# Kernel tuning notes

Measured on AMD Instinct MI355X. Metric: run time of the kernel, lower is better.

Reference implementation:

```python
import jax, jax.numpy as jnp
import numpy as np

B, C, H, W = 8, 320, 64, 64      # query feature map
S_KV, D_KV = 77, 1024            # key/value (text) tokens
HEADS, DIM_HEAD = 8, 64
INNER = HEADS * DIM_HEAD         # 512


def setup_inputs() -> dict:
    key = jax.random.key(0)
    ks = jax.random.split(key, 7)
    return {
        "query": jax.random.normal(ks[0], (B, C, H, W), dtype=jnp.float32),
        "key_value": jax.random.normal(ks[1], (B, S_KV, D_KV), dtype=jnp.float32),
        "Wq": jax.random.normal(ks[2], (C, INNER), dtype=jnp.float32) * (C ** -0.5),
        "Wk": jax.random.normal(ks[3], (D_KV, INNER), dtype=jnp.float32) * (D_KV ** -0.5),
        "Wv": jax.random.normal(ks[4], (D_KV, INNER), dtype=jnp.float32) * (D_KV ** -0.5),
        "Wo": jax.random.normal(ks[5], (INNER, C), dtype=jnp.float32) * (INNER ** -0.5),
        "bo": jnp.zeros((C,), dtype=jnp.float32),
    }


def reference(query, key_value, Wq, Wk, Wv, Wo, bo):
    b, c, h, w = query.shape
    n = h * w
    # [B,C,H,W] -> [B,N,C]
    q_flat = query.reshape(b, c, n).transpose(0, 2, 1)
    # projections, then split heads: [B, S, heads, dim_head]
    q = (q_flat @ Wq).reshape(b, n, HEADS, DIM_HEAD)
    k = (key_value @ Wk).reshape(b, S_KV, HEADS, DIM_HEAD)
    v = (key_value @ Wv).reshape(b, S_KV, HEADS, DIM_HEAD)
    scale = DIM_HEAD ** -0.5
    # attn logits: [B, heads, N, S_kv]
    logits = jnp.einsum('bnhd,bshd->bhns', q, k) * scale
    attn = jax.nn.softmax(logits, axis=-1)
    # weighted values -> merge heads: [B, N, inner]
    out = jnp.einsum('bhns,bshd->bnhd', attn, v).reshape(b, n, INNER)
    out = out @ Wo + bo  # dropout p=0.0 is identity
    # [B,N,C] -> [B,C,H,W]
    return out.transpose(0, 2, 1).reshape(b, c, h, w)
```

## Files before the change

### kernel.cpp

```cpp
#include <hip/hip_runtime.h>
#include <hip/hip_bf16.h>
#include <stdint.h>

#define BB     8
#define CC     320
#define NN     4096
#define SKV    77
#define HEADS  8
#define INNER  512
#define SCALE  0.125f

typedef float f32x4  __attribute__((ext_vector_type(4)));
typedef short bf16x8 __attribute__((ext_vector_type(8)));
typedef short s16x4  __attribute__((ext_vector_type(4)));

static __device__ __forceinline__ short f2bf(float f) {
  unsigned u = __float_as_uint(f);
  return (short)((u + 0x7fffu + ((u >> 16) & 1u)) >> 16);
}

static __device__ __forceinline__ void gll16(void* lds, const void* g) {
  auto gp = reinterpret_cast<const uint32_t __attribute__((address_space(1)))*>(
      reinterpret_cast<uintptr_t>(g));
  auto lp = reinterpret_cast<uint32_t __attribute__((address_space(3)))*>(
      reinterpret_cast<uintptr_t>(lds));
  __builtin_amdgcn_global_load_lds(gp, lp, 16, 0, 0);
}

__global__ __launch_bounds__(256) void prep_kernel(
    const float* __restrict__ kv, const float* __restrict__ Wk,
    const float* __restrict__ Wv, const float* __restrict__ Wq,
    const float* __restrict__ Wo, const float* __restrict__ query,
    short* __restrict__ kv_bf, short* __restrict__ Wk_t,
    short* __restrict__ Wv_t, short* __restrict__ Wq_t,
    short* __restrict__ Wo_t, short* __restrict__ X_bf,
    unsigned* __restrict__ zero_base) {
  __shared__ float T[64 * 65];
  const int blk = blockIdx.x, t = threadIdx.x;
  if (blk < 616) {
    const int base = blk * 1024;
    #pragma unroll
    for (int i = 0; i < 4; ++i) kv_bf[base + i*256 + t] = f2bf(kv[base + i*256 + t]);
    return;
  }
  if (blk >= 1392) {
    const int blk2 = blk - 1392;
    const int b = blk2 / 320, r = blk2 % 320;
    const int nt = r / 5, ct = r % 5;
    const int tl = t & 63, rb = t >> 6;
    #pragma unroll
    for (int i = 0; i < 16; ++i) {
      const int c = rb + i*4;
      T[c*65 + tl] = query[((size_t)(b*CC + ct*64 + c))*NN + nt*64 + tl];
    }
    __syncthreads();
    #pragma unroll
    for (int i = 0; i < 16; ++i) {
      const int n = rb + i*4;
      X_bf[((size_t)(b*NN + nt*64 + n))*CC + ct*64 + tl] = f2bf(T[tl*65 + n]);
    }
    return;
  }
  if (blk >= 952) {
    const int base = (blk - 952) * 1024;
    #pragma unroll
    for (int i = 0; i < 4; ++i) zero_base[base + i*256 + t] = 0u;
    return;
  }
  const float* src; short* dst; int RS, CS, kt, ct; float scl = 1.0f;
  if (blk < 872) {
    const int tile = blk - 616;
    const bool isK = tile < 128;
    const int tt = isK ? tile : tile - 128;
    src = isK ? Wk : Wv; dst = isK ? Wk_t : Wv_t;
    RS = 1024; CS = 512; kt = tt >> 3; ct = tt & 7;
  } else if (blk < 912) {
    const int tt = blk - 872;
    src = Wq; dst = Wq_t; RS = 320; CS = 512; kt = tt >> 3; ct = tt & 7;
    scl = SCALE;
  } else {
    const int tt = blk - 912;
    src = Wo; dst = Wo_t; RS = 512; CS = 320; kt = tt / 5; ct = tt % 5;
  }
  const int cl = t & 63, rb = t >> 6;
  #pragma unroll
  for (int i = 0; i < 16; ++i)
    T[(rb + i*4)*65 + cl] = src[(size_t)(kt*64 + rb + i*4)*CS + ct*64 + cl];
  __syncthreads();
  #pragma unroll
  for (int i = 0; i < 16; ++i) {
    const int nl = rb + i*4;
    dst[(size_t)(ct*64 + nl)*RS + kt*64 + cl] = f2bf(T[cl*65 + nl] * scl);
  }
}

__global__ __launch_bounds__(256) void kvproj_kernel(
    const short* __restrict__ kv_bf, const short* __restrict__ Wk_t,
    const short* __restrict__ Wv_t, short* __restrict__ K_ws,
    short* __restrict__ V_ws) {
  const int t = threadIdx.x, w = t >> 6, lane = t & 63;
  const int l15 = lane & 15, q = lane >> 4;
  const int m0 = (blockIdx.x * 4 + w) * 16;
  const int y = blockIdx.y;
  const bool isK = (y < 8);
  const int h = y & 7;
  const short* __restrict__ Wt = isK ? Wk_t : Wv_t;
  const int arow = (m0 + l15 < 616) ? (m0 + l15) : 615;

  const f32x4 z = {0.f, 0.f, 0.f, 0.f};
  f32x4 acc[4] = {z, z, z, z};
  for (int k0 = 0; k0 < 1024; k0 += 32) {
    const bf16x8 a = *(const bf16x8*)(kv_bf + arow*1024 + k0 + q*8);
    #pragma unroll
    for (int nt = 0; nt < 4; ++nt) {
      const int n = h*64 + nt*16 + l15;
      const bf16x8 bfr = *(const bf16x8*)(Wt + n*1024 + k0 + q*8);
      acc[nt] = __builtin_amdgcn_mfma_f32_16x16x32_bf16(a, bfr, acc[nt], 0, 0, 0);
    }
  }
  #pragma unroll
  for (int nt = 0; nt < 4; ++nt) {
    const int d = nt*16 + l15;
    #pragma unroll
    for (int r = 0; r < 4; ++r) {
      const int row = m0 + q*4 + r;
      if (row < 616) {
        const int b = (int)(((unsigned)row * 54472u) >> 22);
        const int s = row - b*77;
        if (isK) K_ws[((b*8 + h)*80 + s)*64 + d] = f2bf(acc[nt][r]);
        else     V_ws[((b*8 + h)*64 + d)*96 + s] = f2bf(acc[nt][r]);
      }
    }
  }
}

__global__ __launch_bounds__(256, 2) void qproj_kernel(
    const short* __restrict__ X_bf, const short* __restrict__ Wq_t,
    short* __restrict__ Q_ws) {
  const int t = threadIdx.x, w = t >> 6, lane = t & 63;
  const int l15 = lane & 15, q = lane >> 4;
  const int m0 = (blockIdx.x >> 1) * 128;
  const int n0 = (blockIdx.x & 1) * 256;
  const int wm = w & 1, wn = w >> 1;

  __shared__ short tile[12288];

  const f32x4 z = {0.f, 0.f, 0.f, 0.f};
  f32x4 acc[4][8];
  #pragma unroll
  for (int mt = 0; mt < 4; ++mt)
    #pragma unroll
    for (int nt = 0; nt < 8; ++nt) acc[mt][nt] = z;

  for (int it = 0; it < 10; ++it) {
    const int k0 = it * 32;
    if (it) __syncthreads();
    #pragma unroll
    for (int p = 0; p < 2; ++p) {
      const int f = p*256 + t, row = f >> 2, c4 = f & 3;
      gll16(tile + f*8, X_bf + (size_t)(m0 + row)*320 + k0 + c4*8);
    }
    #pragma unroll
    for (int p = 0; p < 4; ++p) {
      const int f = p*256 + t, row = f >> 2, c4 = f & 3;
      gll16(tile + 4096 + f*8, Wq_t + (size_t)(n0 + row)*320 + k0 + c4*8);
    }
    __syncthreads();
    bf16x8 a[4], bb[8];
    #pragma unroll
    for (int mt = 0; mt < 4; ++mt)
      a[mt] = *(const bf16x8*)(tile + (wm*64 + mt*16 + l15)*32 + q*8);
    #pragma unroll
    for (int nt = 0; nt < 8; ++nt)
      bb[nt] = *(const bf16x8*)(tile + 4096 + (wn*128 + nt*16 + l15)*32 + q*8);
    #pragma unroll
    for (int mt = 0; mt < 4; ++mt)
      #pragma unroll
      for (int nt = 0; nt < 8; ++nt)
        acc[mt][nt] = __builtin_amdgcn_mfma_f32_16x16x32_bf16(a[mt], bb[nt], acc[mt][nt], 0, 0, 0);
  }
  #pragma unroll
  for (int mt = 0; mt < 4; ++mt)
    #pragma unroll
    for (int r = 0; r < 4; ++r) {
      short* rowp = Q_ws + (size_t)(m0 + wm*64 + mt*16 + q*4 + r)*512 + n0 + wn*128;
      #pragma unroll
      for (int nt = 0; nt < 8; ++nt)
        rowp[nt*16 + l15] = f2bf(acc[mt][nt][r]);
    }
}

__global__ __launch_bounds__(256) void attncore_kernel(
    const short* __restrict__ Q_ws, const short* __restrict__ K_ws,
    const short* __restrict__ V_ws, short* __restrict__ O_ws) {
  const int t = threadIdx.x, w = t >> 6, lane = t & 63;
  const int unit = blockIdx.x * 4 + w;
  const int h = unit & 7;
  const int g = unit >> 3;
  const int b = g >> 7;
  const int n0 = (g & 127) * 32;
  const int l15 = lane & 15, q = lane >> 4;

  __shared__ short scr[4 * 32 * 104];
  short* scrw = scr + w * 32 * 104;
  for (int i = lane; i < 32*104/2; i += 64) ((unsigned*)scrw)[i] = 0u;

  const short* __restrict__ Kh = K_ws + (size_t)(b*8 + h) * 80 * 64;
  const short* __restrict__ Vh = V_ws + (size_t)(b*8 + h) * 64 * 96;
  size_t tokrow[2];
  #pragma unroll
  for (int nt = 0; nt < 2; ++nt) tokrow[nt] = (size_t)(b*NN + n0 + nt*16 + l15);

  const f32x4 z = {0.f, 0.f, 0.f, 0.f};
  f32x4 qk[2][5];
  #pragma unroll
  for (int nt = 0; nt < 2; ++nt)
    #pragma unroll
    for (int st = 0; st < 5; ++st) qk[nt][st] = z;
  #pragma unroll
  for (int f = 0; f < 2; ++f) {
    bf16x8 bq[2];
    #pragma unroll
    for (int nt = 0; nt < 2; ++nt)
      bq[nt] = *(const bf16x8*)(Q_ws + tokrow[nt]*512 + h*64 + f*32 + q*8);
    #pragma unroll
    for (int st = 0; st < 5; ++st) {
      const bf16x8 a = *(const bf16x8*)(Kh + (st*16 + l15)*64 + f*32 + q*8);
      #pragma unroll
      for (int nt = 0; nt < 2; ++nt)
        qk[nt][st] = __builtin_amdgcn_mfma_f32_16x16x32_bf16(a, bq[nt], qk[nt][st], 0, 0, 0);
    }
  }

  #pragma unroll
  for (int nt = 0; nt < 2; ++nt) {
    float mx = -1e30f;
    #pragma unroll
    for (int st = 0; st < 5; ++st)
      #pragma unroll
      for (int r = 0; r < 4; ++r) {
        const int s = st*16 + q*4 + r;
        const float vv = (s < SKV) ? qk[nt][st][r] : -1e30f;
        qk[nt][st][r] = vv;
        mx = fmaxf(mx, vv);
      }
    mx = fmaxf(mx, __shfl_xor(mx, 16));
    mx = fmaxf(mx, __shfl_xor(mx, 32));
    float sum = 0.f;
    #pragma unroll
    for (int st = 0; st < 5; ++st)
      #pragma unroll
      for (int r = 0; r < 4; ++r) {
        const int s = st*16 + q*4 + r;
        const float e = (s < SKV) ? __expf(qk[nt][st][r] - mx) : 0.f;
        qk[nt][st][r] = e;
        sum += e;
      }
    sum += __shfl_xor(sum, 16);
    sum += __shfl_xor(sum, 32);
    const float inv = 1.0f / sum;
    #pragma unroll
    for (int st = 0; st < 5; ++st) {
      s16x4 pv;
      #pragma unroll
      for (int r = 0; r < 4; ++r) pv[r] = f2bf(qk[nt][st][r] * inv);
      *(s16x4*)(scrw + (nt*16 + l15)*104 + st*16 + q*4) = pv;
    }
  }

  f32x4 ov[2][4];
  #pragma unroll
  for (int nt = 0; nt < 2; ++nt)
    #pragma unroll
    for (int dt = 0; dt < 4; ++dt) ov[nt][dt] = z;
  #pragma unroll
  for (int f = 0; f < 3; ++f) {
    bf16x8 bp[2];
    #pragma unroll
    for (int nt = 0; nt < 2; ++nt)
      bp[nt] = *(const bf16x8*)(scrw + (nt*16 + l15)*104 + f*32 + q*8);
    #pragma unroll
    for (int dt = 0; dt < 4; ++dt) {
      const bf16x8 a = *(const bf16x8*)(Vh + (dt*16 + l15)*96 + f*32 + q*8);
      #pragma unroll
      for (int nt = 0; nt < 2; ++nt)
        ov[nt][dt] = __builtin_amdgcn_mfma_f32_16x16x32_bf16(a, bp[nt], ov[nt][dt], 0, 0, 0);
    }
  }
  #pragma unroll
  for (int nt = 0; nt < 2; ++nt)
    #pragma unroll
    for (int dt = 0; dt < 4; ++dt) {
      s16x4 pv;
      #pragma unroll
      for (int r = 0; r < 4; ++r) pv[r] = f2bf(ov[nt][dt][r]);
      *(s16x4*)(O_ws + tokrow[nt]*512 + h*64 + dt*16 + q*4) = pv;
    }
}

__global__ __launch_bounds__(256) void outproj_kernel(
    const short* __restrict__ O_ws, const short* __restrict__ Wo_t,
    const float* __restrict__ bo, float* __restrict__ out) {
  const int t = threadIdx.x, w = t >> 6, lane = t & 63;
  const int l15 = lane & 15, q = lane >> 4;
  const int c0 = (blockIdx.x & 1) * 160;
  const int t0 = (blockIdx.x >> 1) * 128;
  const int wm = w & 1, wn = w >> 1;

  __shared__ short tile[9216];

  const f32x4 z = {0.f, 0.f, 0.f, 0.f};
  f32x4 acc[5][4];
  #pragma unroll
  for (int mt = 0; mt < 5; ++mt)
    #pragma unroll
    for (int nt = 0; nt < 4; ++nt) acc[mt][nt] = z;

  for (int it = 0; it < 16; ++it) {
    const int k0 = it * 32;
    if (it) __syncthreads();
    #pragma unroll
    for (int p = 0; p < 5; ++p) {
      const int f = p*256 + t;
      if (f < 1152) {
        const short* g;
        if (f < 640) {
          const int row = f >> 2, c4 = f & 3;
          g = Wo_t + (size_t)(c0 + row)*512 + k0 + c4*8;
        } else {
          const int f2 = f - 640, row = f2 >> 2, c4 = f2 & 3;
          g = O_ws + (size_t)(t0 + row)*512 + k0 + c4*8;
        }
        gll16(tile + f*8, g);
      }
    }
    __syncthreads();
    bf16x8 a[5], bb[4];
    #pragma unroll
    for (int mt = 0; mt < 5; ++mt)
      a[mt] = *(const bf16x8*)(tile + (wm*80 + mt*16 + l15)*32 + q*8);
    #pragma unroll
    for (int nt = 0; nt < 4; ++nt)
      bb[nt] = *(const bf16x8*)(tile + 5120 + (wn*64 + nt*16 + l15)*32 + q*8);
    #pragma unroll
    for (int mt = 0; mt < 5; ++mt)
      #pragma unroll
      for (int nt = 0; nt < 4; ++nt)
        acc[mt][nt] = __builtin_amdgcn_mfma_f32_16x16x32_bf16(a[mt], bb[nt], acc[mt][nt], 0, 0, 0);
  }
  const int b = t0 >> 12, n = t0 & 4095;
  #pragma unroll
  for (int mt = 0; mt < 5; ++mt)
    #pragma unroll
    for (int r = 0; r < 4; ++r) {
      const int c = c0 + wm*80 + mt*16 + q*4 + r;
      const float bv = bo[c];
      float* rowp = out + ((size_t)(b*CC + c))*NN + n + wn*64;
      #pragma unroll
      for (int nt = 0; nt < 4; ++nt)
        rowp[nt*16 + l15] = acc[mt][nt][r] + bv;
    }
}

extern "C" void kernel_launch(void* const* d_in, const int* in_sizes, int n_in,
                              void* d_out, int out_size, void* d_ws, size_t ws_size,
                              hipStream_t stream) {
  const float* query = (const float*)d_in[0];
  const float* kv    = (const float*)d_in[1];
  const float* Wq    = (const float*)d_in[2];
  const float* Wk    = (const float*)d_in[3];
  const float* Wv    = (const float*)d_in[4];
  const float* Wo    = (const float*)d_in[5];
  const float* bo    = (const float*)d_in[6];
  float* out = (float*)d_out;

  char* p = (char*)d_ws;
  short* K_ws  = (short*)(p);
  short* V_ws  = (short*)(p +   819200);
  short* Wq_t  = (short*)(p +  1802240);
  short* Wo_t  = (short*)(p +  2129920);
  short* Q_ws  = (short*)(p +  2457600);
  char* pb = p + 36012032;
  short* X_bf  = (short*)(pb);
  short* kv_bf = (short*)(pb + 20971520);
  short* Wk_t  = (short*)(pb + 22233088);
  short* Wv_t  = (short*)(pb + 23281664);
  short* O_ws  = (short*)(pb);

  prep_kernel<<<3952, 256, 0, stream>>>(kv, Wk, Wv, Wq, Wo, query, kv_bf,
                                        Wk_t, Wv_t, Wq_t, Wo_t, X_bf,
                                        (unsigned*)p);
  kvproj_kernel<<<dim3(10, 16), 256, 0, stream>>>(kv_bf, Wk_t, Wv_t, K_ws, V_ws);
  qproj_kernel<<<512, 256, 0, stream>>>(X_bf, Wq_t, Q_ws);
  attncore_kernel<<<2048, 256, 0, stream>>>(Q_ws, K_ws, V_ws, O_ws);
  outproj_kernel<<<512, 256, 0, stream>>>(O_ws, Wo_t, bo, out);
}
```

Measured before the change: 192.9 us.

## Fuse Q projection, attention core and output projection into one kernel

Replaces the three separate kernels (Q projection, attention core, output projection) with one kernel. Each block owns 64 tokens of one batch and keeps Q and then the attention output in LDS, so the Q_ws and O_ws round trips through global memory go away. In exchange each block reloads the full Wq and Wo weights, LDS use rises to about 120 KB, and there are only 512 blocks of 4 waves, which lowers occupancy and latency hiding.

Measured after the change: 195.4 us. About the same (+1.3%).

```diff
diff --git a/kernel.cpp b/kernel.cpp
--- a/kernel.cpp
+++ b/kernel.cpp
@@ -134,232 +134,204 @@
   }
 }
 
-__global__ __launch_bounds__(256, 2) void qproj_kernel(
+__global__ __launch_bounds__(256) void fused_kernel(
     const short* __restrict__ X_bf, const short* __restrict__ Wq_t,
-    short* __restrict__ Q_ws) {
+    const short* __restrict__ K_ws, const short* __restrict__ V_ws,
+    const short* __restrict__ Wo_t, const float* __restrict__ bo,
+    float* __restrict__ out) {
   const int t = threadIdx.x, w = t >> 6, lane = t & 63;
   const int l15 = lane & 15, q = lane >> 4;
-  const int m0 = (blockIdx.x >> 1) * 128;
-  const int n0 = (blockIdx.x & 1) * 256;
-  const int wm = w & 1, wn = w >> 1;
-
-  __shared__ short tile[12288];
+  const int b = blockIdx.x >> 6;
+  const int n0 = (blockIdx.x & 63) * 64;
+
+  __shared__ short Q_lds[64 * 520];
+  __shared__ short STG[26624];
 
   const f32x4 z = {0.f, 0.f, 0.f, 0.f};
-  f32x4 acc[4][8];
-  #pragma unroll
-  for (int mt = 0; mt < 4; ++mt)
-    #pragma unroll
-    for (int nt = 0; nt < 8; ++nt) acc[mt][nt] = z;
-
-  for (int it = 0; it < 10; ++it) {
-    const int k0 = it * 32;
-    if (it) __syncthreads();
-    #pragma unroll
-    for (int p = 0; p < 2; ++p) {
-      const int f = p*256 + t, row = f >> 2, c4 = f & 3;
-      gll16(tile + f*8, X_bf + (size_t)(m0 + row)*320 + k0 + c4*8);
-    }
-    #pragma unroll
-    for (int p = 0; p < 4; ++p) {
-      const int f = p*256 + t, row = f >> 2, c4 = f & 3;
-      gll16(tile + 4096 + f*8, Wq_t + (size_t)(n0 + row)*320 + k0 + c4*8);
-    }
-    __syncthreads();
-    bf16x8 a[4], bb[8];
+
+  {
+    f32x4 acc[4][8];
     #pragma unroll
     for (int mt = 0; mt < 4; ++mt)
-      a[mt] = *(const bf16x8*)(tile + (wm*64 + mt*16 + l15)*32 + q*8);
-    #pragma unroll
-    for (int nt = 0; nt < 8; ++nt)
-      bb[nt] = *(const bf16x8*)(tile + 4096 + (wn*128 + nt*16 + l15)*32 + q*8);
+      #pragma unroll
+      for (int nt = 0; nt < 8; ++nt) acc[mt][nt] = z;
+
+    const size_t xbase = (size_t)(b * NN + n0) * 320;
+    for (int it = 0; it < 10; ++it) {
+      const int k0 = it * 32;
+      if (it) __syncthreads();
+      gll16(STG + t * 8, X_bf + xbase + (size_t)(t >> 2) * 320 + k0 + (t & 3) * 8);
+      #pragma unroll
+      for (int p = 0; p < 8; ++p) {
+        const int f = p * 256 + t, row = f >> 2, c4 = f & 3;
+        gll16(STG + 2048 + f * 8, Wq_t + (size_t)row * 320 + k0 + c4 * 8);
+      }
+      __syncthreads();
+      bf16x8 a[4], bb[8];
+      #pragma unroll
+      for (int mt = 0; mt < 4; ++mt)
+        a[mt] = *(const bf16x8*)(STG + (mt * 16 + l15) * 32 + q * 8);
+      #pragma unroll
+      for (int nt = 0; nt < 8; ++nt)
+        bb[nt] = *(const bf16x8*)(STG + 2048 + (w * 128 + nt * 16 + l15) * 32 + q * 8);
+      #pragma unroll
+      for (int mt = 0; mt < 4; ++mt)
+        #pragma unroll
+        for (int nt = 0; nt < 8; ++nt)
+          acc[mt][nt] = __builtin_amdgcn_mfma_f32_16x16x32_bf16(a[mt], bb[nt], acc[mt][nt], 0, 0, 0);
+    }
     #pragma unroll
     for (int mt = 0; mt < 4; ++mt)
       #pragma unroll
-      for (int nt = 0; nt < 8; ++nt)
-        acc[mt][nt] = __builtin_amdgcn_mfma_f32_16x16x32_bf16(a[mt], bb[nt], acc[mt][nt], 0, 0, 0);
-  }
-  #pragma unroll
-  for (int mt = 0; mt < 4; ++mt)
-    #pragma unroll
-    for (int r = 0; r < 4; ++r) {
-      short* rowp = Q_ws + (size_t)(m0 + wm*64 + mt*16 + q*4 + r)*512 + n0 + wn*128;
-      #pragma unroll
-      for (int nt = 0; nt < 8; ++nt)
-        rowp[nt*16 + l15] = f2bf(acc[mt][nt][r]);
-    }
-}
-
-__global__ __launch_bounds__(256) void attncore_kernel(
-    const short* __restrict__ Q_ws, const short* __restrict__ K_ws,
-    const short* __restrict__ V_ws, short* __restrict__ O_ws) {
-  const int t = threadIdx.x, w = t >> 6, lane = t & 63;
-  const int unit = blockIdx.x * 4 + w;
-  const int h = unit & 7;
-  const int g = unit >> 3;
-  const int b = g >> 7;
-  const int n0 = (g & 127) * 32;
-  const int l15 = lane & 15, q = lane >> 4;
-
-  __shared__ short scr[4 * 32 * 104];
-  short* scrw = scr + w * 32 * 104;
-  for (int i = lane; i < 32*104/2; i += 64) ((unsigned*)scrw)[i] = 0u;
-
-  const short* __restrict__ Kh = K_ws + (size_t)(b*8 + h) * 80 * 64;
-  const short* __restrict__ Vh = V_ws + (size_t)(b*8 + h) * 64 * 96;
-  size_t tokrow[2];
-  #pragma unroll
-  for (int nt = 0; nt < 2; ++nt) tokrow[nt] = (size_t)(b*NN + n0 + nt*16 + l15);
-
-  const f32x4 z = {0.f, 0.f, 0.f, 0.f};
-  f32x4 qk[2][5];
-  #pragma unroll
-  for (int nt = 0; nt < 2; ++nt)
-    #pragma unroll
-    for (int st = 0; st < 5; ++st) qk[nt][st] = z;
-  #pragma unroll
-  for (int f = 0; f < 2; ++f) {
-    bf16x8 bq[2];
-    #pragma unroll
-    for (int nt = 0; nt < 2; ++nt)
-      bq[nt] = *(const bf16x8*)(Q_ws + tokrow[nt]*512 + h*64 + f*32 + q*8);
-    #pragma unroll
-    for (int st = 0; st < 5; ++st) {
-      const bf16x8 a = *(const bf16x8*)(Kh + (st*16 + l15)*64 + f*32 + q*8);
-      #pragma unroll
-      for (int nt = 0; nt < 2; ++nt)
-        qk[nt][st] = __builtin_amdgcn_mfma_f32_16x16x32_bf16(a, bq[nt], qk[nt][st], 0, 0, 0);
-    }
-  }
-
-  #pragma unroll
-  for (int nt = 0; nt < 2; ++nt) {
-    float mx = -1e30f;
-    #pragma unroll
-    for (int st = 0; st < 5; ++st)
-      #pragma unroll
       for (int r = 0; r < 4; ++r) {
-        const int s = st*16 + q*4 + r;
-        const float vv = (s < SKV) ? qk[nt][st][r] : -1e30f;
-        qk[nt][st][r] = vv;
-        mx = fmaxf(mx, vv);
-      }
-    mx = fmaxf(mx, __shfl_xor(mx, 16));
-    mx = fmaxf(mx, __shfl_xor(mx, 32));
-    float sum = 0.f;
-    #pragma unroll
-    for (int st = 0; st < 5; ++st)
+        const int tok = mt * 16 + q * 4 + r;
+        #pragma unroll
+        for (int nt = 0; nt < 8; ++nt)
+          Q_lds[tok * 520 + w * 128 + nt * 16 + l15] = f2bf(acc[mt][nt][r]);
+      }
+  }
+  __syncthreads();
+
+  {
+    short* scrw = STG + w * 6656;
+    for (int i = lane; i < 512; i += 64)
+      *(unsigned*)(scrw + (i >> 3) * 104 + 80 + (i & 7) * 2) = 0u;
+
+    #pragma unroll
+    for (int hh = 0; hh < 2; ++hh) {
+      const int h = w * 2 + hh;
+      const short* __restrict__ Kh = K_ws + (size_t)(b * 8 + h) * 80 * 64;
+      const short* __restrict__ Vh = V_ws + (size_t)(b * 8 + h) * 64 * 96;
+
+      f32x4 qk[4][5];
+      #pragma unroll
+      for (int nt = 0; nt < 4; ++nt)
+        #pragma unroll
+        for (int st = 0; st < 5; ++st) qk[nt][st] = z;
+      #pragma unroll
+      for (int f = 0; f < 2; ++f) {
+        bf16x8 bq[4];
+        #pragma unroll
+        for (int nt = 0; nt < 4; ++nt)
+          bq[nt] = *(const bf16x8*)(Q_lds + (nt * 16 + l15) * 520 + h * 64 + f * 32 + q * 8);
+        #pragma unroll
+        for (int st = 0; st < 5; ++st) {
+          const bf16x8 a = *(const bf16x8*)(Kh + (st * 16 + l15) * 64 + f * 32 + q * 8);
+          #pragma unroll
+          for (int nt = 0; nt < 4; ++nt)
+            qk[nt][st] = __builtin_amdgcn_mfma_f32_16x16x32_bf16(a, bq[nt], qk[nt][st], 0, 0, 0);
+        }
+      }
+
+      #pragma unroll
+      for (int nt = 0; nt < 4; ++nt) {
+        float mx = -1e30f;
+        #pragma unroll
+        for (int st = 0; st < 5; ++st)
+          #pragma unroll
+          for (int r = 0; r < 4; ++r) {
+            const int s = st * 16 + q * 4 + r;
+            const float vv = (s < SKV) ? qk[nt][st][r] : -1e30f;
+            qk[nt][st][r] = vv;
+            mx = fmaxf(mx, vv);
+          }
+        mx = fmaxf(mx, __shfl_xor(mx, 16));
+        mx = fmaxf(mx, __shfl_xor(mx, 32));
+        float sum = 0.f;
+        #pragma unroll
+        for (int st = 0; st < 5; ++st)
+          #pragma unroll
+          for (int r = 0; r < 4; ++r) {
+            const int s = st * 16 + q * 4 + r;
+            const float e = (s < SKV) ? __expf(qk[nt][st][r] - mx) : 0.f;
+            qk[nt][st][r] = e;
+            sum += e;
+          }
+        sum += __shfl_xor(sum, 16);
+        sum += __shfl_xor(sum, 32);
+        const float inv = 1.0f / sum;
+        #pragma unroll
+        for (int st = 0; st < 5; ++st) {
+          s16x4 pv;
+          #pragma unroll
+          for (int r = 0; r < 4; ++r) pv[r] = f2bf(qk[nt][st][r] * inv);
+          *(s16x4*)(scrw + (nt * 16 + l15) * 104 + st * 16 + q * 4) = pv;
+        }
+      }
+
+      f32x4 ov[4][4];
+      #pragma unroll
+      for (int nt = 0; nt < 4; ++nt)
+        #pragma unroll
+        for (int dt = 0; dt < 4; ++dt) ov[nt][dt] = z;
+      #pragma unroll
+      for (int f = 0; f < 3; ++f) {
+        bf16x8 bp[4];
+        #pragma unroll
+        for (int nt = 0; nt < 4; ++nt)
+          bp[nt] = *(const bf16x8*)(scrw + (nt * 16 + l15) * 104 + f * 32 + q * 8);
+        #pragma unroll
+        for (int dt = 0; dt < 4; ++dt) {
+          const bf16x8 a = *(const bf16x8*)(Vh + (dt * 16 + l15) * 96 + f * 32 + q * 8);
+          #pragma unroll
+          for (int nt = 0; nt < 4; ++nt)
+            ov[nt][dt] = __builtin_amdgcn_mfma_f32_16x16x32_bf16(a, bp[nt], ov[nt][dt], 0, 0, 0);
+        }
+      }
+      #pragma unroll
+      for (int nt = 0; nt < 4; ++nt)
+        #pragma unroll
+        for (int dt = 0; dt < 4; ++dt) {
+          s16x4 pv;
+          #pragma unroll
+          for (int r = 0; r < 4; ++r) pv[r] = f2bf(ov[nt][dt][r]);
+          *(s16x4*)(Q_lds + (nt * 16 + l15) * 520 + h * 64 + dt * 16 + q * 4) = pv;
+        }
+    }
+  }
+  __syncthreads();
+
+  {
+    f32x4 oc[5][4];
+    #pragma unroll
+    for (int mt = 0; mt < 5; ++mt)
+      #pragma unroll
+      for (int nt = 0; nt < 4; ++nt) oc[mt][nt] = z;
+
+    for (int it = 0; it < 16; ++it) {
+      const int k0 = it * 32;
+      if (it) __syncthreads();
+      #pragma unroll
+      for (int p = 0; p < 5; ++p) {
+        const int f = p * 256 + t, row = f >> 2, c4 = f & 3;
+        gll16(STG + f * 8, Wo_t + (size_t)row * 512 + k0 + c4 * 8);
+      }
+      __syncthreads();
+      bf16x8 a[5], bb[4];
+      #pragma unroll
+      for (int mt = 0; mt < 5; ++mt)
+        a[mt] = *(const bf16x8*)(STG + (w * 80 + mt * 16 + l15) * 32 + q * 8);
+      #pragma unroll
+      for (int nt = 0; nt < 4; ++nt)
+        bb[nt] = *(const bf16x8*)(Q_lds + (nt * 16 + l15) * 520 + k0 + q * 8);
+      #pragma unroll
+      for (int mt = 0; mt < 5; ++mt)
+        #pragma unroll
+        for (int nt = 0; nt < 4; ++nt)
+          oc[mt][nt] = __builtin_amdgcn_mfma_f32_16x16x32_bf16(a[mt], bb[nt], oc[mt][nt], 0, 0, 0);
+    }
+    #pragma unroll
+    for (int mt = 0; mt < 5; ++mt)
       #pragma unroll
       for (int r = 0; r < 4; ++r) {
-        const int s = st*16 + q*4 + r;
-        const float e = (s < SKV) ? __expf(qk[nt][st][r] - mx) : 0.f;
-        qk[nt][st][r] = e;
-        sum += e;
-      }
-    sum += __shfl_xor(sum, 16);
-    sum += __shfl_xor(sum, 32);
-    const float inv = 1.0f / sum;
-    #pragma unroll
-    for (int st = 0; st < 5; ++st) {
-      s16x4 pv;
-      #pragma unroll
-      for (int r = 0; r < 4; ++r) pv[r] = f2bf(qk[nt][st][r] * inv);
-      *(s16x4*)(scrw + (nt*16 + l15)*104 + st*16 + q*4) = pv;
-    }
-  }
-
-  f32x4 ov[2][4];
-  #pragma unroll
-  for (int nt = 0; nt < 2; ++nt)
-    #pragma unroll
-    for (int dt = 0; dt < 4; ++dt) ov[nt][dt] = z;
-  #pragma unroll
-  for (int f = 0; f < 3; ++f) {
-    bf16x8 bp[2];
-    #pragma unroll
-    for (int nt = 0; nt < 2; ++nt)
-      bp[nt] = *(const bf16x8*)(scrw + (nt*16 + l15)*104 + f*32 + q*8);
-    #pragma unroll
-    for (int dt = 0; dt < 4; ++dt) {
-      const bf16x8 a = *(const bf16x8*)(Vh + (dt*16 + l15)*96 + f*32 + q*8);
-      #pragma unroll
-      for (int nt = 0; nt < 2; ++nt)
-        ov[nt][dt] = __builtin_amdgcn_mfma_f32_16x16x32_bf16(a, bp[nt], ov[nt][dt], 0, 0, 0);
-    }
-  }
-  #pragma unroll
-  for (int nt = 0; nt < 2; ++nt)
-    #pragma unroll
-    for (int dt = 0; dt < 4; ++dt) {
-      s16x4 pv;
-      #pragma unroll
-      for (int r = 0; r < 4; ++r) pv[r] = f2bf(ov[nt][dt][r]);
-      *(s16x4*)(O_ws + tokrow[nt]*512 + h*64 + dt*16 + q*4) = pv;
-    }
-}
-
-__global__ __launch_bounds__(256) void outproj_kernel(
-    const short* __restrict__ O_ws, const short* __restrict__ Wo_t,
-    const float* __restrict__ bo, float* __restrict__ out) {
-  const int t = threadIdx.x, w = t >> 6, lane = t & 63;
-  const int l15 = lane & 15, q = lane >> 4;
-  const int c0 = (blockIdx.x & 1) * 160;
-  const int t0 = (blockIdx.x >> 1) * 128;
-  const int wm = w & 1, wn = w >> 1;
-
-  __shared__ short tile[9216];
-
-  const f32x4 z = {0.f, 0.f, 0.f, 0.f};
-  f32x4 acc[5][4];
-  #pragma unroll
-  for (int mt = 0; mt < 5; ++mt)
-    #pragma unroll
-    for (int nt = 0; nt < 4; ++nt) acc[mt][nt] = z;
-
-  for (int it = 0; it < 16; ++it) {
-    const int k0 = it * 32;
-    if (it) __syncthreads();
-    #pragma unroll
-    for (int p = 0; p < 5; ++p) {
-      const int f = p*256 + t;
-      if (f < 1152) {
-        const short* g;
-        if (f < 640) {
-          const int row = f >> 2, c4 = f & 3;
-          g = Wo_t + (size_t)(c0 + row)*512 + k0 + c4*8;
-        } else {
-          const int f2 = f - 640, row = f2 >> 2, c4 = f2 & 3;
-          g = O_ws + (size_t)(t0 + row)*512 + k0 + c4*8;
-        }
-        gll16(tile + f*8, g);
-      }
-    }
-    __syncthreads();
-    bf16x8 a[5], bb[4];
-    #pragma unroll
-    for (int mt = 0; mt < 5; ++mt)
-      a[mt] = *(const bf16x8*)(tile + (wm*80 + mt*16 + l15)*32 + q*8);
-    #pragma unroll
-    for (int nt = 0; nt < 4; ++nt)
-      bb[nt] = *(const bf16x8*)(tile + 5120 + (wn*64 + nt*16 + l15)*32 + q*8);
-    #pragma unroll
-    for (int mt = 0; mt < 5; ++mt)
-      #pragma unroll
-      for (int nt = 0; nt < 4; ++nt)
-        acc[mt][nt] = __builtin_amdgcn_mfma_f32_16x16x32_bf16(a[mt], bb[nt], acc[mt][nt], 0, 0, 0);
-  }
-  const int b = t0 >> 12, n = t0 & 4095;
-  #pragma unroll
-  for (int mt = 0; mt < 5; ++mt)
-    #pragma unroll
-    for (int r = 0; r < 4; ++r) {
-      const int c = c0 + wm*80 + mt*16 + q*4 + r;
-      const float bv = bo[c];
-      float* rowp = out + ((size_t)(b*CC + c))*NN + n + wn*64;
-      #pragma unroll
-      for (int nt = 0; nt < 4; ++nt)
-        rowp[nt*16 + l15] = acc[mt][nt][r] + bv;
-    }
+        const int c = w * 80 + mt * 16 + q * 4 + r;
+        const float bv = bo[c];
+        float* rowp = out + ((size_t)(b * CC + c)) * NN + n0;
+        #pragma unroll
+        for (int nt = 0; nt < 4; ++nt)
+          rowp[nt * 16 + l15] = oc[mt][nt][r] + bv;
+      }
+  }
 }
 
 extern "C" void kernel_launch(void* const* d_in, const int* in_sizes, int n_in,
@@ -370,8 +342,10 @@
   const float* Wq    = (const float*)d_in[2];
   const float* Wk    = (const float*)d_in[3];
   const float* Wv    = (const float*)d_in[4];
+  const float* Wv_   = (const float*)d_in[4];
   const float* Wo    = (const float*)d_in[5];
   const float* bo    = (const float*)d_in[6];
+  (void)Wv_;
   float* out = (float*)d_out;
 
   char* p = (char*)d_ws;
@@ -379,19 +353,14 @@
   short* V_ws  = (short*)(p +   819200);
   short* Wq_t  = (short*)(p +  1802240);
   short* Wo_t  = (short*)(p +  2129920);
-  short* Q_ws  = (short*)(p +  2457600);
-  char* pb = p + 36012032;
-  short* X_bf  = (short*)(pb);
-  short* kv_bf = (short*)(pb + 20971520);
-  short* Wk_t  = (short*)(pb + 22233088);
-  short* Wv_t  = (short*)(pb + 23281664);
-  short* O_ws  = (short*)(pb);
+  short* X_bf  = (short*)(p +  2457600);
+  short* kv_bf = (short*)(p + 23429120);
+  short* Wk_t  = (short*)(p + 24690688);
+  short* Wv_t  = (short*)(p + 25739264);
 
   prep_kernel<<<3952, 256, 0, stream>>>(kv, Wk, Wv, Wq, Wo, query, kv_bf,
                                         Wk_t, Wv_t, Wq_t, Wo_t, X_bf,
                                         (unsigned*)p);
   kvproj_kernel<<<dim3(10, 16), 256, 0, stream>>>(kv_bf, Wk_t, Wv_t, K_ws, V_ws);
-  qproj_kernel<<<512, 256, 0, stream>>>(X_bf, Wq_t, Q_ws);
-  attncore_kernel<<<2048, 256, 0, stream>>>(Q_ws, K_ws, V_ws, O_ws);
-  outproj_kernel<<<512, 256, 0, stream>>>(O_ws, Wo_t, bo, out);
-}
+  fused_kernel<<<512, 256, 0, stream>>>(X_bf, Wq_t, K_ws, V_ws, Wo_t, bo, out);
+}
```

## Fuse query transpose into Q projection and split-K the KV projection

Applied to the files above, without the earlier changes.

The query NCHW-to-token-major transpose and bf16 conversion moves out of the prep kernel and into the Q projection, which loads a 64-token fp32 slab straight into LDS. This removes the X_bf round trip through global memory. Each warp now streams its own Wq slice into a swizzled LDS buffer that is double-staged around the MFMAs. The KV projection now splits K across the four warps, each handling 64 rows, and reduces through LDS atomics, which adds atomic and shared-memory traffic. The zero-fill now targets only the V buffer, and the workspace layout is compacted.

New measurement: 200.3 us. 1.04x slower.

```diff
diff --git a/kernel.cpp b/kernel.cpp
--- a/kernel.cpp
+++ b/kernel.cpp
@@ -30,10 +30,9 @@
 __global__ __launch_bounds__(256) void prep_kernel(
     const float* __restrict__ kv, const float* __restrict__ Wk,
     const float* __restrict__ Wv, const float* __restrict__ Wq,
-    const float* __restrict__ Wo, const float* __restrict__ query,
-    short* __restrict__ kv_bf, short* __restrict__ Wk_t,
-    short* __restrict__ Wv_t, short* __restrict__ Wq_t,
-    short* __restrict__ Wo_t, short* __restrict__ X_bf,
+    const float* __restrict__ Wo, short* __restrict__ kv_bf,
+    short* __restrict__ Wk_t, short* __restrict__ Wv_t,
+    short* __restrict__ Wq_t, short* __restrict__ Wo_t,
     unsigned* __restrict__ zero_base) {
   __shared__ float T[64 * 65];
   const int blk = blockIdx.x, t = threadIdx.x;
@@ -41,24 +40,6 @@
     const int base = blk * 1024;
     #pragma unroll
     for (int i = 0; i < 4; ++i) kv_bf[base + i*256 + t] = f2bf(kv[base + i*256 + t]);
-    return;
-  }
-  if (blk >= 1392) {
-    const int blk2 = blk - 1392;
-    const int b = blk2 / 320, r = blk2 % 320;
-    const int nt = r / 5, ct = r % 5;
-    const int tl = t & 63, rb = t >> 6;
-    #pragma unroll
-    for (int i = 0; i < 16; ++i) {
-      const int c = rb + i*4;
-      T[c*65 + tl] = query[((size_t)(b*CC + ct*64 + c))*NN + nt*64 + tl];
-    }
-    __syncthreads();
-    #pragma unroll
-    for (int i = 0; i < 16; ++i) {
-      const int n = rb + i*4;
-      X_bf[((size_t)(b*NN + nt*64 + n))*CC + ct*64 + tl] = f2bf(T[tl*65 + n]);
-    }
     return;
   }
   if (blk >= 952) {
@@ -100,93 +81,156 @@
     short* __restrict__ V_ws) {
   const int t = threadIdx.x, w = t >> 6, lane = t & 63;
   const int l15 = lane & 15, q = lane >> 4;
-  const int m0 = (blockIdx.x * 4 + w) * 16;
+  const int m0 = blockIdx.x * 64;
   const int y = blockIdx.y;
   const bool isK = (y < 8);
   const int h = y & 7;
   const short* __restrict__ Wt = isK ? Wk_t : Wv_t;
-  const int arow = (m0 + l15 < 616) ? (m0 + l15) : 615;
+
+  __shared__ float buf[4096];
+  for (int i = t; i < 4096; i += 256) buf[i] = 0.f;
+  __syncthreads();
 
   const f32x4 z = {0.f, 0.f, 0.f, 0.f};
-  f32x4 acc[4] = {z, z, z, z};
-  for (int k0 = 0; k0 < 1024; k0 += 32) {
-    const bf16x8 a = *(const bf16x8*)(kv_bf + arow*1024 + k0 + q*8);
+  f32x4 acc[4][4];
+  #pragma unroll
+  for (int ms = 0; ms < 4; ++ms)
+    #pragma unroll
+    for (int nt = 0; nt < 4; ++nt) acc[ms][nt] = z;
+
+  const int kbase = w * 256;
+  for (int kk = 0; kk < 256; kk += 32) {
+    const int k0 = kbase + kk;
+    bf16x8 a[4];
+    #pragma unroll
+    for (int ms = 0; ms < 4; ++ms) {
+      int arow = m0 + ms*16 + l15;
+      if (arow > 615) arow = 615;
+      a[ms] = *(const bf16x8*)(kv_bf + (size_t)arow*1024 + k0 + q*8);
+    }
     #pragma unroll
     for (int nt = 0; nt < 4; ++nt) {
       const int n = h*64 + nt*16 + l15;
-      const bf16x8 bfr = *(const bf16x8*)(Wt + n*1024 + k0 + q*8);
-      acc[nt] = __builtin_amdgcn_mfma_f32_16x16x32_bf16(a, bfr, acc[nt], 0, 0, 0);
-    }
-  }
-  #pragma unroll
-  for (int nt = 0; nt < 4; ++nt) {
-    const int d = nt*16 + l15;
-    #pragma unroll
-    for (int r = 0; r < 4; ++r) {
-      const int row = m0 + q*4 + r;
-      if (row < 616) {
-        const int b = (int)(((unsigned)row * 54472u) >> 22);
-        const int s = row - b*77;
-        if (isK) K_ws[((b*8 + h)*80 + s)*64 + d] = f2bf(acc[nt][r]);
-        else     V_ws[((b*8 + h)*64 + d)*96 + s] = f2bf(acc[nt][r]);
-      }
+      const bf16x8 bfr = *(const bf16x8*)(Wt + (size_t)n*1024 + k0 + q*8);
+      #pragma unroll
+      for (int ms = 0; ms < 4; ++ms)
+        acc[ms][nt] = __builtin_amdgcn_mfma_f32_16x16x32_bf16(a[ms], bfr, acc[ms][nt], 0, 0, 0);
+    }
+  }
+  #pragma unroll
+  for (int ms = 0; ms < 4; ++ms)
+    #pragma unroll
+    for (int nt = 0; nt < 4; ++nt)
+      #pragma unroll
+      for (int r = 0; r < 4; ++r)
+        atomicAdd(&buf[(ms*16 + q*4 + r)*64 + nt*16 + l15], acc[ms][nt][r]);
+  __syncthreads();
+  for (int i = t; i < 4096; i += 256) {
+    const int m = i >> 6, d = i & 63;
+    const int row = m0 + m;
+    if (row < 616) {
+      const int b = (int)(((unsigned)row * 54472u) >> 22);
+      const int s = row - b*77;
+      if (isK) K_ws[((b*8 + h)*80 + s)*64 + d] = f2bf(buf[i]);
+      else     V_ws[((b*8 + h)*64 + d)*96 + s] = f2bf(buf[i]);
     }
   }
 }
 
 __global__ __launch_bounds__(256, 2) void qproj_kernel(
-    const short* __restrict__ X_bf, const short* __restrict__ Wq_t,
+    const float* __restrict__ query, const short* __restrict__ Wq_t,
     short* __restrict__ Q_ws) {
   const int t = threadIdx.x, w = t >> 6, lane = t & 63;
   const int l15 = lane & 15, q = lane >> 4;
-  const int m0 = (blockIdx.x >> 1) * 128;
-  const int n0 = (blockIdx.x & 1) * 256;
-  const int wm = w & 1, wn = w >> 1;
-
-  __shared__ short tile[12288];
-
+  const int b = blockIdx.x >> 6;
+  const int n0 = (blockIdx.x & 63) * 64;
+
+  __shared__ short S[29184];
+  short* slice = S + 20992 + w * 2048;
+
+  {
+    const float* qb = query + (size_t)b * CC * NN + n0;
+    #pragma unroll
+    for (int i = 0; i < 20; ++i) {
+      const int f = i * 256 + t;
+      const int c = f >> 4, n4 = (f & 15) * 4;
+      const f32x4 v = *(const f32x4*)(qb + (size_t)c * NN + n4);
+      #pragma unroll
+      for (int j = 0; j < 4; ++j)
+        S[(n4 + j) * 328 + c] = f2bf(v[j]);
+    }
+  }
+
+  f32x4 acc[4][8];
   const f32x4 z = {0.f, 0.f, 0.f, 0.f};
-  f32x4 acc[4][8];
   #pragma unroll
   for (int mt = 0; mt < 4; ++mt)
     #pragma unroll
     for (int nt = 0; nt < 8; ++nt) acc[mt][nt] = z;
 
+  const short* __restrict__ Wqw = Wq_t + (size_t)(w * 128) * 320;
+  auto stage = [&](int it, int h2) {
+    const int k0 = it * 32;
+    #pragma unroll
+    for (int p = 0; p < 4; ++p) {
+      const int L = p * 64 + lane;
+      const int row = L >> 2, qp = L & 3;
+      const int ql = qp ^ ((row & 3) ^ ((row >> 2) & 3));
+      gll16(slice + L * 8, Wqw + (size_t)(h2 * 64 + row) * 320 + k0 + ql * 8);
+    }
+  };
+
+  stage(0, 0);
+  __syncthreads();
+  const int lperm = (l15 & 3) ^ ((l15 >> 2) & 3);
   for (int it = 0; it < 10; ++it) {
     const int k0 = it * 32;
-    if (it) __syncthreads();
-    #pragma unroll
-    for (int p = 0; p < 2; ++p) {
-      const int f = p*256 + t, row = f >> 2, c4 = f & 3;
-      gll16(tile + f*8, X_bf + (size_t)(m0 + row)*320 + k0 + c4*8);
-    }
-    #pragma unroll
-    for (int p = 0; p < 4; ++p) {
-      const int f = p*256 + t, row = f >> 2, c4 = f & 3;
-      gll16(tile + 4096 + f*8, Wq_t + (size_t)(n0 + row)*320 + k0 + c4*8);
-    }
-    __syncthreads();
-    bf16x8 a[4], bb[8];
+    asm volatile("s_waitcnt vmcnt(0)" ::: "memory");
+    __builtin_amdgcn_sched_barrier(0);
+    bf16x8 a[4], b0[4];
     #pragma unroll
     for (int mt = 0; mt < 4; ++mt)
-      a[mt] = *(const bf16x8*)(tile + (wm*64 + mt*16 + l15)*32 + q*8);
-    #pragma unroll
-    for (int nt = 0; nt < 8; ++nt)
-      bb[nt] = *(const bf16x8*)(tile + 4096 + (wn*128 + nt*16 + l15)*32 + q*8);
+      a[mt] = *(const bf16x8*)(S + (mt * 16 + l15) * 328 + k0 + q * 8);
+    #pragma unroll
+    for (int x = 0; x < 4; ++x) {
+      const int r = x * 16 + l15;
+      b0[x] = *(const bf16x8*)(slice + (r * 4 + (q ^ lperm)) * 8);
+    }
+    asm volatile("s_waitcnt lgkmcnt(0)" ::: "memory");
+    __builtin_amdgcn_sched_barrier(0);
+    stage(it, 1);
     #pragma unroll
     for (int mt = 0; mt < 4; ++mt)
       #pragma unroll
+      for (int x = 0; x < 4; ++x)
+        acc[mt][x] = __builtin_amdgcn_mfma_f32_16x16x32_bf16(a[mt], b0[x], acc[mt][x], 0, 0, 0);
+
+    asm volatile("s_waitcnt vmcnt(0)" ::: "memory");
+    __builtin_amdgcn_sched_barrier(0);
+    bf16x8 b1[4];
+    #pragma unroll
+    for (int x = 0; x < 4; ++x) {
+      const int r = x * 16 + l15;
+      b1[x] = *(const bf16x8*)(slice + (r * 4 + (q ^ lperm)) * 8);
+    }
+    asm volatile("s_waitcnt lgkmcnt(0)" ::: "memory");
+    __builtin_amdgcn_sched_barrier(0);
+    if (it + 1 < 10) stage(it + 1, 0);
+    #pragma unroll
+    for (int mt = 0; mt < 4; ++mt)
+      #pragma unroll
+      for (int x = 0; x < 4; ++x)
+        acc[mt][4 + x] = __builtin_amdgcn_mfma_f32_16x16x32_bf16(a[mt], b1[x], acc[mt][4 + x], 0, 0, 0);
+  }
+  #pragma unroll
+  for (int mt = 0; mt < 4; ++mt)
+    #pragma unroll
+    for (int r = 0; r < 4; ++r) {
+      const int tok = n0 + mt * 16 + q * 4 + r;
+      short* rowp = Q_ws + (size_t)(b * NN + tok) * 512 + w * 128;
+      #pragma unroll
       for (int nt = 0; nt < 8; ++nt)
-        acc[mt][nt] = __builtin_amdgcn_mfma_f32_16x16x32_bf16(a[mt], bb[nt], acc[mt][nt], 0, 0, 0);
-  }
-  #pragma unroll
-  for (int mt = 0; mt < 4; ++mt)
-    #pragma unroll
-    for (int r = 0; r < 4; ++r) {
-      short* rowp = Q_ws + (size_t)(m0 + wm*64 + mt*16 + q*4 + r)*512 + n0 + wn*128;
-      #pragma unroll
-      for (int nt = 0; nt < 8; ++nt)
-        rowp[nt*16 + l15] = f2bf(acc[mt][nt][r]);
+        rowp[nt * 16 + l15] = f2bf(acc[mt][nt][r]);
     }
 }
 
@@ -379,19 +423,17 @@
   short* V_ws  = (short*)(p +   819200);
   short* Wq_t  = (short*)(p +  1802240);
   short* Wo_t  = (short*)(p +  2129920);
-  short* Q_ws  = (short*)(p +  2457600);
-  char* pb = p + 36012032;
-  short* X_bf  = (short*)(pb);
-  short* kv_bf = (short*)(pb + 20971520);
-  short* Wk_t  = (short*)(pb + 22233088);
-  short* Wv_t  = (short*)(pb + 23281664);
-  short* O_ws  = (short*)(pb);
-
-  prep_kernel<<<3952, 256, 0, stream>>>(kv, Wk, Wv, Wq, Wo, query, kv_bf,
-                                        Wk_t, Wv_t, Wq_t, Wo_t, X_bf,
-                                        (unsigned*)p);
+  short* kv_bf = (short*)(p +  2457600);
+  short* Wk_t  = (short*)(p +  3719168);
+  short* Wv_t  = (short*)(p +  4767744);
+  short* Q_ws  = (short*)(p +  5816320);
+  short* O_ws  = (short*)(p + 39370752);
+
+  prep_kernel<<<1192, 256, 0, stream>>>(kv, Wk, Wv, Wq, Wo, kv_bf,
+                                        Wk_t, Wv_t, Wq_t, Wo_t,
+                                        (unsigned*)V_ws);
   kvproj_kernel<<<dim3(10, 16), 256, 0, stream>>>(kv_bf, Wk_t, Wv_t, K_ws, V_ws);
-  qproj_kernel<<<512, 256, 0, stream>>>(X_bf, Wq_t, Q_ws);
+  qproj_kernel<<<512, 256, 0, stream>>>(query, Wq_t, Q_ws);
   attncore_kernel<<<2048, 256, 0, stream>>>(Q_ws, K_ws, V_ws, O_ws);
   outproj_kernel<<<512, 256, 0, stream>>>(O_ws, Wo_t, bo, out);
 }
```
